# Kernel optimization log

Measured on AMD Instinct MI355X. Metric: run time of the kernel, lower is better.

## Reference

```python
import jax, jax.numpy as jnp
import numpy as np

DIM = 180
HEADS = 6
HEAD_DIM = DIM // HEADS
SCALE = HEAD_DIM ** (-0.5)
BW, N, K = 8192, 64, 16


def setup_inputs() -> dict:
    key = jax.random.key(0)
    ks = jax.random.split(key, 6)
    return {
        "x": jax.random.normal(ks[0], (BW, N, DIM), dtype=jnp.float32),
        "bpe_windows": jax.random.normal(ks[1], (BW, N, K), dtype=jnp.float32),
        "qkv_w": jax.random.normal(ks[2], (3 * DIM, DIM), dtype=jnp.float32) * 0.05,
        "qkv_b": jax.random.normal(ks[3], (3 * DIM,), dtype=jnp.float32) * 0.05,
        "proj_w": jax.random.normal(ks[4], (DIM, DIM), dtype=jnp.float32) * 0.05,
        "proj_b": jax.random.normal(ks[5], (DIM,), dtype=jnp.float32) * 0.05,
        "tau": jnp.ones((HEADS, 1, 1), dtype=jnp.float32),
    }


def reference(x, bpe_windows, qkv_w, qkv_b, proj_w, proj_b, tau):
    B_, n, C = x.shape
    # qkv projection -> (3, B_, H, N, hd)
    qkv = (x @ qkv_w.T + qkv_b).reshape(B_, n, 3, HEADS, HEAD_DIM)
    qkv = jnp.transpose(qkv, (2, 0, 3, 1, 4))
    q, k, v = qkv[0], qkv[1], qkv[2]
    q = q * SCALE
    attn = jnp.einsum("bhid,bhjd->bhij", q, k)  # (B_, H, N, N)
    # geodesic bias from BPE embeddings: d_B(i,j) = ||bpe_i - bpe_j||_2
    diff = bpe_windows[:, :, None, :] - bpe_windows[:, None, :, :]  # (B_, N, N, K)
    d_B = jnp.sqrt(jnp.sum(diff * diff, axis=-1))  # (B_, N, N)
    log_W_geo = -d_B[:, None, :, :] / jnp.clip(tau, 1e-6)[None]  # (B_, H, N, N)
    attn = jax.nn.softmax(attn + log_W_geo, axis=-1)
    out = jnp.einsum("bhij,bhjd->bhid", attn, v)  # (B_, H, N, hd)
    out = jnp.transpose(out, (0, 2, 1, 3)).reshape(B_, n, C)
    return out @ proj_w.T + proj_b
```

## Files before the change

kernel.cpp:

```cpp
#include <hip/hip_runtime.h>
#include <math.h>

typedef __attribute__((ext_vector_type(8))) short short8b;
typedef __attribute__((ext_vector_type(4))) float f32x4;
typedef __attribute__((ext_vector_type(4))) unsigned short ushort4b;

#define NWIN 8192
#define NT   1024
#define SCALE 0.18257418583505536f

#define XB_P 200
#define QK_P 392
#define VT_P 72
#define DB_P 66

#define OFF_XB  0
#define OFF_QK  25600
#define OFF_VT  75776
#define OFF_DB  103424
#define OFF_BPE 120320
#define LDS_BYTES 125440

#define WK 192

__device__ __forceinline__ unsigned short f2bf(float f) {
    union { float f; unsigned int u; } v; v.f = f;
    return (unsigned short)((v.u + 0x7FFFu + ((v.u >> 16) & 1u)) >> 16);
}

__global__ void prep_weights(const float* __restrict__ qkv_w,
                             const float* __restrict__ proj_w,
                             unsigned short* __restrict__ wqr,
                             unsigned short* __restrict__ wpr)
{
    const int idx = blockIdx.x * 256 + threadIdx.x;
    if (idx < 540 * WK) {
        const int r = idx / WK, k = idx % WK;
        const int seg = r / 30, dd = r % 30;
        const int which = seg / 6, hh = seg % 6;
        float v = 0.f;
        if (k < 180)
            v = qkv_w[(which * 180 + hh * 30 + dd) * 180 + k];
        wqr[idx] = f2bf(v);
    }
    const int j = idx - 540 * WK;
    if (j >= 0 && j < WK * WK) {
        const int r = j / WK, kp = j % WK;
        const int hh = kp >> 5, dd = kp & 31;
        float v = 0.f;
        if (r < 180 && dd < 30)
            v = proj_w[r * 180 + hh * 30 + dd];
        wpr[j] = f2bf(v);
    }
}

__global__ void __launch_bounds__(NT, 4)
waga_mfma(const float* __restrict__ x,
          const float* __restrict__ bpe,
          const unsigned short* __restrict__ wqr,
          const unsigned short* __restrict__ wpr,
          const float* __restrict__ qkv_b,
          const float* __restrict__ proj_b,
          const float* __restrict__ tau,
          float* __restrict__ out)
{
    extern __shared__ char smem[];
    unsigned short* xb   = (unsigned short*)(smem + OFF_XB);
    unsigned short* qk   = (unsigned short*)(smem + OFF_QK);
    unsigned short* vT   = (unsigned short*)(smem + OFF_VT);
    float*          dBs  = (float*)(smem + OFF_DB);
    float*          bpes = (float*)(smem + OFF_BPE);
    unsigned short* att  = xb;

    const int b = blockIdx.x;
    const int t = threadIdx.x;
    const int w = t >> 6;
    const int l = t & 63;
    const int lr = l & 15;
    const int g  = l >> 4;

    if (t < 192) {
        const int n = t / 3, c = t % 3;
        *reinterpret_cast<uint2*>(xb + n * XB_P + 180 + 4 * c) = make_uint2(0u, 0u);
    }
    {
        const float* xw = x + (size_t)b * 11520;
        for (int i = t; i < 64 * 45; i += NT) {
            const int n = i / 45, c4 = i % 45;
            const float4 v = *reinterpret_cast<const float4*>(xw + i * 4);
            ushort4b o;
            o[0] = f2bf(v.x); o[1] = f2bf(v.y); o[2] = f2bf(v.z); o[3] = f2bf(v.w);
            *reinterpret_cast<ushort4b*>(xb + n * XB_P + c4 * 4) = o;
        }
    }
    if (t < 256) {
        const float4 v = *reinterpret_cast<const float4*>(bpe + (size_t)b * 1024 + t * 4);
        *reinterpret_cast<float4*>(bpes + (t >> 2) * 20 + (t & 3) * 4) = v;
    }
    __syncthreads();

    {
        const int ti = t >> 4, tj = t & 15;
        float acc[4] = {0.f, 0.f, 0.f, 0.f};
        #pragma unroll
        for (int k4 = 0; k4 < 4; ++k4) {
            const float4 a = *reinterpret_cast<const float4*>(bpes + ti * 20 + 4 * k4);
            #pragma unroll
            for (int e = 0; e < 4; ++e) {
                const float4 bb = *reinterpret_cast<const float4*>(bpes + (tj + 16 * e) * 20 + 4 * k4);
                float d;
                d = a.x - bb.x; acc[e] += d * d;
                d = a.y - bb.y; acc[e] += d * d;
                d = a.z - bb.z; acc[e] += d * d;
                d = a.w - bb.w; acc[e] += d * d;
            }
        }
        #pragma unroll
        for (int e = 0; e < 4; ++e)
            dBs[ti * DB_P + tj + 16 * e] = sqrtf(acc[e]);
    }

    for (int tile = w; tile < 36; tile += 16) {
        const int seg = tile >> 1, half = tile & 1;
        const int which = seg / 6, hh = seg % 6;
        const int ddr = half * 16 + lr;
        const bool arow_ok = (ddr < 30);
        const unsigned short* wrow = wqr + (size_t)(seg * 30 + (arow_ok ? ddr : 0)) * WK;
        short8b wf[6];
        #pragma unroll
        for (int kk = 0; kk < 6; ++kk) {
            if (arow_ok)
                wf[kk] = *reinterpret_cast<const short8b*>(wrow + kk * 32 + g * 8);
            else
                wf[kk] = short8b{0, 0, 0, 0, 0, 0, 0, 0};
        }
        const int ddb = half * 16 + g * 4;
        const int cbase = which * 180 + hh * 30;
        f32x4 binit;
        #pragma unroll
        for (int i = 0; i < 4; ++i)
            binit[i] = (ddb + i < 30) ? qkv_b[cbase + ddb + i] : 0.f;
        f32x4 acc[4] = {binit, binit, binit, binit};
        short8b xf[4];
        #pragma unroll
        for (int mt = 0; mt < 4; ++mt)
            xf[mt] = *reinterpret_cast<const short8b*>(xb + (mt * 16 + lr) * XB_P + g * 8);
        #pragma unroll
        for (int kk = 0; kk < 6; ++kk) {
            short8b xc[4];
            #pragma unroll
            for (int mt = 0; mt < 4; ++mt) xc[mt] = xf[mt];
            if (kk < 5) {
                #pragma unroll
                for (int mt = 0; mt < 4; ++mt)
                    xf[mt] = *reinterpret_cast<const short8b*>(
                        xb + (mt * 16 + lr) * XB_P + (kk + 1) * 32 + g * 8);
            }
            #pragma unroll
            for (int mt = 0; mt < 4; ++mt)
                acc[mt] = __builtin_amdgcn_mfma_f32_16x16x32_bf16(wf[kk], xc[mt], acc[mt], 0, 0, 0);
        }
        #pragma unroll
        for (int mt = 0; mt < 4; ++mt) {
            const int tok = mt * 16 + lr;
            float v0 = acc[mt][0], v1 = acc[mt][1], v2 = acc[mt][2], v3 = acc[mt][3];
            if (which == 0) { v0 *= SCALE; v1 *= SCALE; v2 *= SCALE; v3 *= SCALE; }
            if (which < 2) {
                ushort4b o;
                o[0] = f2bf(v0); o[1] = f2bf(v1); o[2] = f2bf(v2); o[3] = f2bf(v3);
                *reinterpret_cast<ushort4b*>(qk + tok * QK_P + hh * 64 + which * 32 + ddb) = o;
            } else {
                const int c = (tok & 32) + ((tok >> 2) & 3) * 8 + ((tok >> 4) & 1) * 4 + (tok & 3);
                unsigned short* vb = vT + hh * 2304 + ddb * VT_P + c;
                vb[0 * VT_P] = f2bf(v0);
                vb[1 * VT_P] = f2bf(v1);
                vb[2 * VT_P] = f2bf(v2);
                vb[3 * VT_P] = f2bf(v3);
            }
        }
    }
    __syncthreads();

    for (int u = w; u < 24; u += 16) {
        const int h = u >> 2, mt = u & 3;
        const unsigned short* qkh = qk + h * 64;
        const short8b qf = *reinterpret_cast<const short8b*>(qkh + (mt * 16 + lr) * QK_P + g * 8);
        short8b kf[4];
        #pragma unroll
        for (int jt = 0; jt < 4; ++jt)
            kf[jt] = *reinterpret_cast<const short8b*>(qkh + (jt * 16 + lr) * QK_P + 32 + g * 8);
        short8b vf[2][2];
        #pragma unroll
        for (int ntd = 0; ntd < 2; ++ntd)
            #pragma unroll
            for (int ks = 0; ks < 2; ++ks)
                vf[ntd][ks] = *reinterpret_cast<const short8b*>(
                    vT + h * 2304 + (ntd * 16 + lr) * VT_P + ks * 32 + g * 8);
        const float itau = 1.f / fmaxf(tau[h], 1e-6f);
        f32x4 s[4];
        #pragma unroll
        for (int jt = 0; jt < 4; ++jt)
            #pragma unroll
            for (int i = 0; i < 4; ++i)
                s[jt][i] = -itau * dBs[(jt * 16 + g * 4 + i) * DB_P + mt * 16 + lr];
        #pragma unroll
        for (int jt = 0; jt < 4; ++jt)
            s[jt] = __builtin_amdgcn_mfma_f32_16x16x32_bf16(kf[jt], qf, s[jt], 0, 0, 0);
        float mx = s[0][0];
        #pragma unroll
        for (int jt = 0; jt < 4; ++jt)
            #pragma unroll
            for (int i = 0; i < 4; ++i) mx = fmaxf(mx, s[jt][i]);
        mx = fmaxf(mx, __shfl_xor(mx, 16));
        mx = fmaxf(mx, __shfl_xor(mx, 32));
        float sum = 0.f;
        #pragma unroll
        for (int jt = 0; jt < 4; ++jt)
            #pragma unroll
            for (int i = 0; i < 4; ++i) {
                const float p = __expf(s[jt][i] - mx);
                s[jt][i] = p; sum += p;
            }
        sum += __shfl_xor(sum, 16);
        sum += __shfl_xor(sum, 32);
        const float inv = 1.f / sum;
        short8b pb[2];
        #pragma unroll
        for (int ks = 0; ks < 2; ++ks) {
            pb[ks][0] = (short)f2bf(s[2 * ks][0] * inv);
            pb[ks][1] = (short)f2bf(s[2 * ks][1] * inv);
            pb[ks][2] = (short)f2bf(s[2 * ks][2] * inv);
            pb[ks][3] = (short)f2bf(s[2 * ks][3] * inv);
            pb[ks][4] = (short)f2bf(s[2 * ks + 1][0] * inv);
            pb[ks][5] = (short)f2bf(s[2 * ks + 1][1] * inv);
            pb[ks][6] = (short)f2bf(s[2 * ks + 1][2] * inv);
            pb[ks][7] = (short)f2bf(s[2 * ks + 1][3] * inv);
        }
        const int tok = mt * 16 + lr;
        #pragma unroll
        for (int ntd = 0; ntd < 2; ++ntd) {
            f32x4 o = {0.f, 0.f, 0.f, 0.f};
            o = __builtin_amdgcn_mfma_f32_16x16x32_bf16(vf[ntd][0], pb[0], o, 0, 0, 0);
            o = __builtin_amdgcn_mfma_f32_16x16x32_bf16(vf[ntd][1], pb[1], o, 0, 0, 0);
            ushort4b ov;
            ov[0] = f2bf(o[0]); ov[1] = f2bf(o[1]); ov[2] = f2bf(o[2]); ov[3] = f2bf(o[3]);
            *reinterpret_cast<ushort4b*>(att + tok * XB_P + h * 32 + ntd * 16 + g * 4) = ov;
        }
    }
    __syncthreads();

    {
        const int mt = w & 3, ntb = w >> 2;
        short8b attf[6];
        #pragma unroll
        for (int kk = 0; kk < 6; ++kk)
            attf[kk] = *reinterpret_cast<const short8b*>(
                att + (mt * 16 + lr) * XB_P + kk * 32 + g * 8);
        #pragma unroll
        for (int q3 = 0; q3 < 3; ++q3) {
            const int nt = ntb + 4 * q3;
            const unsigned short* wrow = wpr + (size_t)(nt * 16 + lr) * WK;
            short8b wf[6];
            #pragma unroll
            for (int kk = 0; kk < 6; ++kk)
                wf[kk] = *reinterpret_cast<const short8b*>(wrow + kk * 32 + g * 8);
            const int cb = nt * 16 + g * 4;
            f32x4 acc;
            #pragma unroll
            for (int i = 0; i < 4; ++i)
                acc[i] = (cb + i < 180) ? proj_b[cb + i] : 0.f;
            #pragma unroll
            for (int kk = 0; kk < 6; ++kk)
                acc = __builtin_amdgcn_mfma_f32_16x16x32_bf16(wf[kk], attf[kk], acc, 0, 0, 0);
            if (cb < 177) {
                const int tok = mt * 16 + lr;
                *reinterpret_cast<float4*>(out + ((size_t)b * 64 + tok) * 180 + cb) =
                    make_float4(acc[0], acc[1], acc[2], acc[3]);
            }
        }
    }
}

extern "C" void kernel_launch(void* const* d_in, const int* in_sizes, int n_in,
                              void* d_out, int out_size, void* d_ws, size_t ws_size,
                              hipStream_t stream) {
    (void)in_sizes; (void)n_in; (void)out_size; (void)ws_size;
    const float* x      = (const float*)d_in[0];
    const float* bpe    = (const float*)d_in[1];
    const float* qkv_w  = (const float*)d_in[2];
    const float* qkv_b  = (const float*)d_in[3];
    const float* proj_w = (const float*)d_in[4];
    const float* proj_b = (const float*)d_in[5];
    const float* tau    = (const float*)d_in[6];

    unsigned short* wqr = (unsigned short*)d_ws;
    unsigned short* wpr = wqr + 540 * WK;

    prep_weights<<<(540 * WK + WK * WK + 255) / 256, 256, 0, stream>>>(
        qkv_w, proj_w, wqr, wpr);

    (void)hipFuncSetAttribute((const void*)waga_mfma,
                              hipFuncAttributeMaxDynamicSharedMemorySize,
                              LDS_BYTES);
    waga_mfma<<<NWIN, NT, LDS_BYTES, stream>>>(x, bpe, wqr, wpr, qkv_b, proj_b, tau,
                                               (float*)d_out);
}
```

Baseline: 745.1 us.

## Halve block size and LDS footprint by processing heads in two passes

Result: faster. 728.5 us (-2.2%).

```diff
diff --git a/kernel.cpp b/kernel.cpp
--- a/kernel.cpp
+++ b/kernel.cpp
@@ -1,25 +1,28 @@
 #include <hip/hip_runtime.h>
+#include <hip/hip_fp16.h>
 #include <math.h>
 
 typedef __attribute__((ext_vector_type(8))) short short8b;
 typedef __attribute__((ext_vector_type(4))) float f32x4;
 typedef __attribute__((ext_vector_type(4))) unsigned short ushort4b;
+typedef __attribute__((ext_vector_type(2))) unsigned short ushort2b;
 
 #define NWIN 8192
-#define NT   1024
+#define NT   512
 #define SCALE 0.18257418583505536f
 
 #define XB_P 200
-#define QK_P 392
+#define QK_P 200
 #define VT_P 72
-#define DB_P 66
+#define DB_P 68
+#define ATT_P 184
 
 #define OFF_XB  0
 #define OFF_QK  25600
-#define OFF_VT  75776
-#define OFF_DB  103424
-#define OFF_BPE 120320
-#define LDS_BYTES 125440
+#define OFF_VT  51200
+#define OFF_DB  65024
+#define OFF_BPE 73728
+#define LDS_BYTES 78848
 
 #define WK 192
 
@@ -45,11 +48,10 @@
     }
     const int j = idx - 540 * WK;
     if (j >= 0 && j < WK * WK) {
-        const int r = j / WK, kp = j % WK;
-        const int hh = kp >> 5, dd = kp & 31;
+        const int r = j / WK, k = j % WK;
         float v = 0.f;
-        if (r < 180 && dd < 30)
-            v = proj_w[r * 180 + hh * 30 + dd];
+        if (r < 180 && k < 180)
+            v = proj_w[r * 180 + k];
         wpr[j] = f2bf(v);
     }
 }
@@ -68,9 +70,8 @@
     unsigned short* xb   = (unsigned short*)(smem + OFF_XB);
     unsigned short* qk   = (unsigned short*)(smem + OFF_QK);
     unsigned short* vT   = (unsigned short*)(smem + OFF_VT);
-    float*          dBs  = (float*)(smem + OFF_DB);
+    unsigned short* dBs  = (unsigned short*)(smem + OFF_DB);
     float*          bpes = (float*)(smem + OFF_BPE);
-    unsigned short* att  = xb;
 
     const int b = blockIdx.x;
     const int t = threadIdx.x;
@@ -79,9 +80,15 @@
     const int lr = l & 15;
     const int g  = l >> 4;
 
+    unsigned short* attg = (unsigned short*)((char*)out + (size_t)b * 46080 + 22528);
+
     if (t < 192) {
         const int n = t / 3, c = t % 3;
         *reinterpret_cast<uint2*>(xb + n * XB_P + 180 + 4 * c) = make_uint2(0u, 0u);
+    } else if (t < 256) {
+        const int n = t - 192;
+        ushort4b z = {0, 0, 0, 0};
+        *reinterpret_cast<ushort4b*>(attg + n * ATT_P + 180) = z;
     }
     {
         const float* xw = x + (size_t)b * 11520;
@@ -101,181 +108,237 @@
 
     {
         const int ti = t >> 4, tj = t & 15;
-        float acc[4] = {0.f, 0.f, 0.f, 0.f};
+        float acc0[4] = {0.f, 0.f, 0.f, 0.f};
+        float acc1[4] = {0.f, 0.f, 0.f, 0.f};
         #pragma unroll
         for (int k4 = 0; k4 < 4; ++k4) {
-            const float4 a = *reinterpret_cast<const float4*>(bpes + ti * 20 + 4 * k4);
+            const float4 a0 = *reinterpret_cast<const float4*>(bpes + ti * 20 + 4 * k4);
+            const float4 a1 = *reinterpret_cast<const float4*>(bpes + (ti + 32) * 20 + 4 * k4);
             #pragma unroll
             for (int e = 0; e < 4; ++e) {
                 const float4 bb = *reinterpret_cast<const float4*>(bpes + (tj + 16 * e) * 20 + 4 * k4);
                 float d;
-                d = a.x - bb.x; acc[e] += d * d;
-                d = a.y - bb.y; acc[e] += d * d;
-                d = a.z - bb.z; acc[e] += d * d;
-                d = a.w - bb.w; acc[e] += d * d;
-            }
-        }
-        #pragma unroll
-        for (int e = 0; e < 4; ++e)
-            dBs[ti * DB_P + tj + 16 * e] = sqrtf(acc[e]);
-    }
-
-    for (int tile = w; tile < 36; tile += 16) {
-        const int seg = tile >> 1, half = tile & 1;
-        const int which = seg / 6, hh = seg % 6;
-        const int ddr = half * 16 + lr;
-        const bool arow_ok = (ddr < 30);
-        const unsigned short* wrow = wqr + (size_t)(seg * 30 + (arow_ok ? ddr : 0)) * WK;
-        short8b wf[6];
-        #pragma unroll
-        for (int kk = 0; kk < 6; ++kk) {
-            if (arow_ok)
-                wf[kk] = *reinterpret_cast<const short8b*>(wrow + kk * 32 + g * 8);
-            else
-                wf[kk] = short8b{0, 0, 0, 0, 0, 0, 0, 0};
-        }
-        const int ddb = half * 16 + g * 4;
-        const int cbase = which * 180 + hh * 30;
-        f32x4 binit;
-        #pragma unroll
-        for (int i = 0; i < 4; ++i)
-            binit[i] = (ddb + i < 30) ? qkv_b[cbase + ddb + i] : 0.f;
-        f32x4 acc[4] = {binit, binit, binit, binit};
-        short8b xf[4];
-        #pragma unroll
-        for (int mt = 0; mt < 4; ++mt)
-            xf[mt] = *reinterpret_cast<const short8b*>(xb + (mt * 16 + lr) * XB_P + g * 8);
-        #pragma unroll
-        for (int kk = 0; kk < 6; ++kk) {
-            short8b xc[4];
-            #pragma unroll
-            for (int mt = 0; mt < 4; ++mt) xc[mt] = xf[mt];
-            if (kk < 5) {
+                d = a0.x - bb.x; acc0[e] += d * d;
+                d = a0.y - bb.y; acc0[e] += d * d;
+                d = a0.z - bb.z; acc0[e] += d * d;
+                d = a0.w - bb.w; acc0[e] += d * d;
+                d = a1.x - bb.x; acc1[e] += d * d;
+                d = a1.y - bb.y; acc1[e] += d * d;
+                d = a1.z - bb.z; acc1[e] += d * d;
+                d = a1.w - bb.w; acc1[e] += d * d;
+            }
+        }
+        #pragma unroll
+        for (int e = 0; e < 4; ++e) {
+            dBs[ti * DB_P + tj + 16 * e] =
+                __half_as_ushort(__float2half_rn(sqrtf(acc0[e])));
+            dBs[(ti + 32) * DB_P + tj + 16 * e] =
+                __half_as_ushort(__float2half_rn(sqrtf(acc1[e])));
+        }
+    }
+
+    for (int pass = 0; pass < 2; ++pass) {
+        if (pass) __syncthreads();
+
+        {
+            f32x4 acc[3][4];
+            const unsigned short* wrow[3];
+            bool has[3], arow_ok[3];
+            int whichv[3], hhl[3], halfv[3];
+            #pragma unroll
+            for (int ti = 0; ti < 3; ++ti) {
+                const int tl = w + 8 * ti;
+                has[ti] = (tl < 18);
+                const int tls = has[ti] ? tl : 0;
+                const int segl = tls >> 1;
+                halfv[ti] = tls & 1;
+                whichv[ti] = segl / 3;
+                hhl[ti] = segl % 3;
+                const int hg = 3 * pass + hhl[ti];
+                const int wseg = whichv[ti] * 6 + hg;
+                const int ddr = halfv[ti] * 16 + lr;
+                arow_ok[ti] = (ddr < 30);
+                wrow[ti] = wqr + (size_t)(wseg * 30 + (arow_ok[ti] ? ddr : 0)) * WK;
+                const int ddb = halfv[ti] * 16 + g * 4;
+                const int cbase = whichv[ti] * 180 + hg * 30;
+                f32x4 binit;
+                #pragma unroll
+                for (int i = 0; i < 4; ++i)
+                    binit[i] = (ddb + i < 30) ? qkv_b[cbase + ddb + i] : 0.f;
+                #pragma unroll
+                for (int mt = 0; mt < 4; ++mt) acc[ti][mt] = binit;
+            }
+            #pragma unroll
+            for (int kk = 0; kk < 6; ++kk) {
+                short8b xf[4];
                 #pragma unroll
                 for (int mt = 0; mt < 4; ++mt)
                     xf[mt] = *reinterpret_cast<const short8b*>(
-                        xb + (mt * 16 + lr) * XB_P + (kk + 1) * 32 + g * 8);
-            }
-            #pragma unroll
-            for (int mt = 0; mt < 4; ++mt)
-                acc[mt] = __builtin_amdgcn_mfma_f32_16x16x32_bf16(wf[kk], xc[mt], acc[mt], 0, 0, 0);
-        }
-        #pragma unroll
-        for (int mt = 0; mt < 4; ++mt) {
+                        xb + (mt * 16 + lr) * XB_P + kk * 32 + g * 8);
+                #pragma unroll
+                for (int ti = 0; ti < 3; ++ti) {
+                    if (!has[ti]) continue;
+                    short8b wfv;
+                    if (arow_ok[ti])
+                        wfv = *reinterpret_cast<const short8b*>(wrow[ti] + kk * 32 + g * 8);
+                    else
+                        wfv = short8b{0, 0, 0, 0, 0, 0, 0, 0};
+                    #pragma unroll
+                    for (int mt = 0; mt < 4; ++mt)
+                        acc[ti][mt] = __builtin_amdgcn_mfma_f32_16x16x32_bf16(
+                            wfv, xf[mt], acc[ti][mt], 0, 0, 0);
+                }
+            }
+            #pragma unroll
+            for (int ti = 0; ti < 3; ++ti) {
+                if (!has[ti]) continue;
+                const int ddb = halfv[ti] * 16 + g * 4;
+                #pragma unroll
+                for (int mt = 0; mt < 4; ++mt) {
+                    const int tok = mt * 16 + lr;
+                    float v0 = acc[ti][mt][0], v1 = acc[ti][mt][1];
+                    float v2 = acc[ti][mt][2], v3 = acc[ti][mt][3];
+                    if (whichv[ti] == 0) { v0 *= SCALE; v1 *= SCALE; v2 *= SCALE; v3 *= SCALE; }
+                    if (whichv[ti] < 2) {
+                        ushort4b o;
+                        o[0] = f2bf(v0); o[1] = f2bf(v1); o[2] = f2bf(v2); o[3] = f2bf(v3);
+                        *reinterpret_cast<ushort4b*>(
+                            qk + tok * QK_P + hhl[ti] * 64 + whichv[ti] * 32 + ddb) = o;
+                    } else {
+                        const int c = (tok & 32) + ((tok >> 2) & 3) * 8 + ((tok >> 4) & 1) * 4 + (tok & 3);
+                        unsigned short* vb = vT + hhl[ti] * 2304 + ddb * VT_P + c;
+                        vb[0 * VT_P] = f2bf(v0);
+                        vb[1 * VT_P] = f2bf(v1);
+                        vb[2 * VT_P] = f2bf(v2);
+                        vb[3 * VT_P] = f2bf(v3);
+                    }
+                }
+            }
+        }
+        __syncthreads();
+
+        for (int u = w; u < 12; u += 8) {
+            const int hh = u >> 2, mt = u & 3;
+            const int h = 3 * pass + hh;
+            const unsigned short* qkh = qk + hh * 64;
+            const short8b qf = *reinterpret_cast<const short8b*>(
+                qkh + (mt * 16 + lr) * QK_P + g * 8);
+            short8b kf[4];
+            #pragma unroll
+            for (int jt = 0; jt < 4; ++jt)
+                kf[jt] = *reinterpret_cast<const short8b*>(
+                    qkh + (jt * 16 + lr) * QK_P + 32 + g * 8);
+            short8b vf[2][2];
+            #pragma unroll
+            for (int ntd = 0; ntd < 2; ++ntd)
+                #pragma unroll
+                for (int ks = 0; ks < 2; ++ks)
+                    vf[ntd][ks] = *reinterpret_cast<const short8b*>(
+                        vT + hh * 2304 + (ntd * 16 + lr) * VT_P + ks * 32 + g * 8);
+            const float itau = 1.f / fmaxf(tau[h], 1e-6f);
+            f32x4 s[4];
+            #pragma unroll
+            for (int jt = 0; jt < 4; ++jt) {
+                const ushort4b du = *reinterpret_cast<const ushort4b*>(
+                    dBs + (mt * 16 + lr) * DB_P + jt * 16 + g * 4);
+                #pragma unroll
+                for (int i = 0; i < 4; ++i)
+                    s[jt][i] = -itau * __half2float(__ushort_as_half(du[i]));
+            }
+            #pragma unroll
+            for (int jt = 0; jt < 4; ++jt)
+                s[jt] = __builtin_amdgcn_mfma_f32_16x16x32_bf16(kf[jt], qf, s[jt], 0, 0, 0);
+            float mx = s[0][0];
+            #pragma unroll
+            for (int jt = 0; jt < 4; ++jt)
+                #pragma unroll
+                for (int i = 0; i < 4; ++i) mx = fmaxf(mx, s[jt][i]);
+            mx = fmaxf(mx, __shfl_xor(mx, 16));
+            mx = fmaxf(mx, __shfl_xor(mx, 32));
+            float sum = 0.f;
+            #pragma unroll
+            for (int jt = 0; jt < 4; ++jt)
+                #pragma unroll
+                for (int i = 0; i < 4; ++i) {
+                    const float p = __expf(s[jt][i] - mx);
+                    s[jt][i] = p; sum += p;
+                }
+            sum += __shfl_xor(sum, 16);
+            sum += __shfl_xor(sum, 32);
+            const float inv = 1.f / sum;
+            short8b pb[2];
+            #pragma unroll
+            for (int ks = 0; ks < 2; ++ks) {
+                pb[ks][0] = (short)f2bf(s[2 * ks][0] * inv);
+                pb[ks][1] = (short)f2bf(s[2 * ks][1] * inv);
+                pb[ks][2] = (short)f2bf(s[2 * ks][2] * inv);
+                pb[ks][3] = (short)f2bf(s[2 * ks][3] * inv);
+                pb[ks][4] = (short)f2bf(s[2 * ks + 1][0] * inv);
+                pb[ks][5] = (short)f2bf(s[2 * ks + 1][1] * inv);
+                pb[ks][6] = (short)f2bf(s[2 * ks + 1][2] * inv);
+                pb[ks][7] = (short)f2bf(s[2 * ks + 1][3] * inv);
+            }
             const int tok = mt * 16 + lr;
-            float v0 = acc[mt][0], v1 = acc[mt][1], v2 = acc[mt][2], v3 = acc[mt][3];
-            if (which == 0) { v0 *= SCALE; v1 *= SCALE; v2 *= SCALE; v3 *= SCALE; }
-            if (which < 2) {
-                ushort4b o;
-                o[0] = f2bf(v0); o[1] = f2bf(v1); o[2] = f2bf(v2); o[3] = f2bf(v3);
-                *reinterpret_cast<ushort4b*>(qk + tok * QK_P + hh * 64 + which * 32 + ddb) = o;
-            } else {
-                const int c = (tok & 32) + ((tok >> 2) & 3) * 8 + ((tok >> 4) & 1) * 4 + (tok & 3);
-                unsigned short* vb = vT + hh * 2304 + ddb * VT_P + c;
-                vb[0 * VT_P] = f2bf(v0);
-                vb[1 * VT_P] = f2bf(v1);
-                vb[2 * VT_P] = f2bf(v2);
-                vb[3 * VT_P] = f2bf(v3);
+            #pragma unroll
+            for (int ntd = 0; ntd < 2; ++ntd) {
+                f32x4 o = {0.f, 0.f, 0.f, 0.f};
+                o = __builtin_amdgcn_mfma_f32_16x16x32_bf16(vf[ntd][0], pb[0], o, 0, 0, 0);
+                o = __builtin_amdgcn_mfma_f32_16x16x32_bf16(vf[ntd][1], pb[1], o, 0, 0, 0);
+                const int col = h * 30 + ntd * 16 + g * 4;
+                unsigned short* dst = attg + tok * ATT_P + col;
+                if (ntd == 0 || g < 3) {
+                    ushort4b ov;
+                    ov[0] = f2bf(o[0]); ov[1] = f2bf(o[1]);
+                    ov[2] = f2bf(o[2]); ov[3] = f2bf(o[3]);
+                    *reinterpret_cast<ushort4b*>(dst) = ov;
+                } else {
+                    ushort2b ov;
+                    ov[0] = f2bf(o[0]); ov[1] = f2bf(o[1]);
+                    *reinterpret_cast<ushort2b*>(dst) = ov;
+                }
             }
         }
     }
     __syncthreads();
 
-    for (int u = w; u < 24; u += 16) {
-        const int h = u >> 2, mt = u & 3;
-        const unsigned short* qkh = qk + h * 64;
-        const short8b qf = *reinterpret_cast<const short8b*>(qkh + (mt * 16 + lr) * QK_P + g * 8);
-        short8b kf[4];
-        #pragma unroll
-        for (int jt = 0; jt < 4; ++jt)
-            kf[jt] = *reinterpret_cast<const short8b*>(qkh + (jt * 16 + lr) * QK_P + 32 + g * 8);
-        short8b vf[2][2];
-        #pragma unroll
-        for (int ntd = 0; ntd < 2; ++ntd)
-            #pragma unroll
-            for (int ks = 0; ks < 2; ++ks)
-                vf[ntd][ks] = *reinterpret_cast<const short8b*>(
-                    vT + h * 2304 + (ntd * 16 + lr) * VT_P + ks * 32 + g * 8);
-        const float itau = 1.f / fmaxf(tau[h], 1e-6f);
-        f32x4 s[4];
-        #pragma unroll
-        for (int jt = 0; jt < 4; ++jt)
-            #pragma unroll
-            for (int i = 0; i < 4; ++i)
-                s[jt][i] = -itau * dBs[(jt * 16 + g * 4 + i) * DB_P + mt * 16 + lr];
-        #pragma unroll
-        for (int jt = 0; jt < 4; ++jt)
-            s[jt] = __builtin_amdgcn_mfma_f32_16x16x32_bf16(kf[jt], qf, s[jt], 0, 0, 0);
-        float mx = s[0][0];
-        #pragma unroll
-        for (int jt = 0; jt < 4; ++jt)
-            #pragma unroll
-            for (int i = 0; i < 4; ++i) mx = fmaxf(mx, s[jt][i]);
-        mx = fmaxf(mx, __shfl_xor(mx, 16));
-        mx = fmaxf(mx, __shfl_xor(mx, 32));
-        float sum = 0.f;
-        #pragma unroll
-        for (int jt = 0; jt < 4; ++jt)
-            #pragma unroll
-            for (int i = 0; i < 4; ++i) {
-                const float p = __expf(s[jt][i] - mx);
-                s[jt][i] = p; sum += p;
-            }
-        sum += __shfl_xor(sum, 16);
-        sum += __shfl_xor(sum, 32);
-        const float inv = 1.f / sum;
-        short8b pb[2];
-        #pragma unroll
-        for (int ks = 0; ks < 2; ++ks) {
-            pb[ks][0] = (short)f2bf(s[2 * ks][0] * inv);
-            pb[ks][1] = (short)f2bf(s[2 * ks][1] * inv);
-            pb[ks][2] = (short)f2bf(s[2 * ks][2] * inv);
-            pb[ks][3] = (short)f2bf(s[2 * ks][3] * inv);
-            pb[ks][4] = (short)f2bf(s[2 * ks + 1][0] * inv);
-            pb[ks][5] = (short)f2bf(s[2 * ks + 1][1] * inv);
-            pb[ks][6] = (short)f2bf(s[2 * ks + 1][2] * inv);
-            pb[ks][7] = (short)f2bf(s[2 * ks + 1][3] * inv);
-        }
-        const int tok = mt * 16 + lr;
-        #pragma unroll
-        for (int ntd = 0; ntd < 2; ++ntd) {
-            f32x4 o = {0.f, 0.f, 0.f, 0.f};
-            o = __builtin_amdgcn_mfma_f32_16x16x32_bf16(vf[ntd][0], pb[0], o, 0, 0, 0);
-            o = __builtin_amdgcn_mfma_f32_16x16x32_bf16(vf[ntd][1], pb[1], o, 0, 0, 0);
-            ushort4b ov;
-            ov[0] = f2bf(o[0]); ov[1] = f2bf(o[1]); ov[2] = f2bf(o[2]); ov[3] = f2bf(o[3]);
-            *reinterpret_cast<ushort4b*>(att + tok * XB_P + h * 32 + ntd * 16 + g * 4) = ov;
-        }
-    }
-    __syncthreads();
-
     {
-        const int mt = w & 3, ntb = w >> 2;
+        const int mt = w & 3;
+        const int ntb = (w >> 2) * 6;
         short8b attf[6];
         #pragma unroll
-        for (int kk = 0; kk < 6; ++kk)
-            attf[kk] = *reinterpret_cast<const short8b*>(
-                att + (mt * 16 + lr) * XB_P + kk * 32 + g * 8);
-        #pragma unroll
-        for (int q3 = 0; q3 < 3; ++q3) {
-            const int nt = ntb + 4 * q3;
+        for (int kk = 0; kk < 6; ++kk) {
+            if (kk == 5 && g == 3)
+                attf[kk] = short8b{0, 0, 0, 0, 0, 0, 0, 0};
+            else
+                attf[kk] = *reinterpret_cast<const short8b*>(
+                    attg + (mt * 16 + lr) * ATT_P + kk * 32 + g * 8);
+        }
+        f32x4 pacc[6];
+        #pragma unroll
+        for (int q6 = 0; q6 < 6; ++q6) {
+            const int nt = ntb + q6;
             const unsigned short* wrow = wpr + (size_t)(nt * 16 + lr) * WK;
-            short8b wf[6];
-            #pragma unroll
-            for (int kk = 0; kk < 6; ++kk)
-                wf[kk] = *reinterpret_cast<const short8b*>(wrow + kk * 32 + g * 8);
             const int cb = nt * 16 + g * 4;
             f32x4 acc;
             #pragma unroll
             for (int i = 0; i < 4; ++i)
                 acc[i] = (cb + i < 180) ? proj_b[cb + i] : 0.f;
             #pragma unroll
-            for (int kk = 0; kk < 6; ++kk)
-                acc = __builtin_amdgcn_mfma_f32_16x16x32_bf16(wf[kk], attf[kk], acc, 0, 0, 0);
+            for (int kk = 0; kk < 6; ++kk) {
+                const short8b wf = *reinterpret_cast<const short8b*>(wrow + kk * 32 + g * 8);
+                acc = __builtin_amdgcn_mfma_f32_16x16x32_bf16(wf, attf[kk], acc, 0, 0, 0);
+            }
+            pacc[q6] = acc;
+        }
+        __syncthreads();
+        #pragma unroll
+        for (int q6 = 0; q6 < 6; ++q6) {
+            const int nt = ntb + q6;
+            const int cb = nt * 16 + g * 4;
             if (cb < 177) {
                 const int tok = mt * 16 + lr;
                 *reinterpret_cast<float4*>(out + ((size_t)b * 64 + tok) * 180 + cb) =
-                    make_float4(acc[0], acc[1], acc[2], acc[3]);
+                    make_float4(pacc[q6][0], pacc[q6][1], pacc[q6][2], pacc[q6][3]);
             }
         }
     }
```
